# Kernel tuning notes

Measured on AMD Instinct MI355X. Metric: run time of the kernel, lower is better.

## Reference

```python
import jax, jax.numpy as jnp
import numpy as np

ATTN_DIM = 64

def setup_inputs() -> dict:
    key = jax.random.key(0)
    k1, k2, k3, k4, k5 = jax.random.split(key, 5)
    B, S, E, D = 4, 2048, 16, 256
    return {
        "input_gate": jax.random.uniform(k1, (B, S, E, 1), dtype=jnp.float32),
        "q_expert_vector": jax.random.normal(k2, (B, S, E, D), dtype=jnp.float32),
        "k_expert_vector": jax.random.normal(k3, (B, S, E, D), dtype=jnp.float32),
        "Wq": jax.random.normal(k4, (D, ATTN_DIM), dtype=jnp.float32) * 0.02,
        "Wk": jax.random.normal(k5, (D, ATTN_DIM), dtype=jnp.float32) * 0.02,
    }

def reference(input_gate, q_expert_vector, k_expert_vector, Wq, Wk):
    # project: (B,S,E,D) @ (D,A) -> (B,S,E,A)
    query = jnp.einsum("bsed,da->bsea", q_expert_vector, Wq)
    key = jnp.einsum("bsed,da->bsea", k_expert_vector, Wk)
    # attention over experts: (B,S,E,E)
    sim = jnp.einsum("bsqa,bska->bsqk", query, key) / jnp.sqrt(
        jnp.asarray(ATTN_DIM, dtype=query.dtype))
    sim = jax.nn.softmax(sim, axis=-1)
    # gate: (B,S,E,E) @ (B,S,E,1) -> (B,S,E,1)
    gate = jnp.matmul(sim, input_gate)
    routing_weight = jax.nn.softmax(gate.squeeze(-1), axis=-1)  # (B,S,E)
    return routing_weight
```

## Files before the change

kernel.cpp:

```cpp
#include <hip/hip_runtime.h>
#include <hip/hip_bf16.h>

typedef __attribute__((ext_vector_type(8))) short short8;
typedef __attribute__((ext_vector_type(4))) float f32x4;

#define WPB 8
#define BLOCK 512
#define W_PITCH 528
#define W_MAT (64 * W_PITCH)
#define QK_PITCH 144
#define QK_TILE (16 * QK_PITCH)
#define LDS_W (2 * W_MAT)
#define SCR_PW (4 * QK_TILE)
#define LDS_TOTAL (LDS_W + WPB * SCR_PW)

union S8U { short8 s; unsigned u[4]; };

__device__ __forceinline__ unsigned pk2(float a, float b) {
  __hip_bfloat162 h = __float22bfloat162_rn(make_float2(a, b));
  return *reinterpret_cast<unsigned*>(&h);
}
__device__ __forceinline__ unsigned short bf1(float a) {
  __hip_bfloat16 h = __float2bfloat16(a);
  return *reinterpret_cast<unsigned short*>(&h);
}

#define LOADX(BUF, KS) {                                                      \
  _Pragma("unroll") for (int t = 0; t < 4; ++t) {                             \
    BUF[t][0] = *(const float4*)(xr[t] + (KS) * 32);                          \
    BUF[t][1] = *(const float4*)(xr[t] + (KS) * 32 + 4);                      \
  } }

#define STEP(BUF, KS, WLDS, ACC) {                                            \
  short8 af[4];                                                               \
  _Pragma("unroll") for (int t = 0; t < 4; ++t) {                             \
    S8U u_;                                                                   \
    u_.u[0] = pk2(BUF[t][0].x, BUF[t][0].y);                                  \
    u_.u[1] = pk2(BUF[t][0].z, BUF[t][0].w);                                  \
    u_.u[2] = pk2(BUF[t][1].x, BUF[t][1].y);                                  \
    u_.u[3] = pk2(BUF[t][1].z, BUF[t][1].w);                                  \
    af[t] = u_.s;                                                             \
  }                                                                           \
  _Pragma("unroll") for (int n = 0; n < 4; ++n) {                             \
    short8 bfr = *(const short8*)((WLDS) + (n * 16 + e) * W_PITCH + (KS) * 64 + g * 16); \
    _Pragma("unroll") for (int t = 0; t < 4; ++t)                             \
      ACC[t][n] = __builtin_amdgcn_mfma_f32_16x16x32_bf16(af[t], bfr, ACC[t][n], 0, 0, 0); \
  } }

#define PROJ_PASS(XBASE, WLDS, ACC) {                                         \
  const float* xr[4];                                                         \
  _Pragma("unroll") for (int t = 0; t < 4; ++t)                               \
    xr[t] = (XBASE) + (size_t)tk[t] * 4096 + e * 256 + g * 8;                 \
  float4 b0[4][2], b1[4][2];                                                  \
  LOADX(b0, 0); LOADX(b1, 1);                                                 \
  _Pragma("unroll") for (int kp = 0; kp < 4; ++kp) {                          \
    STEP(b0, 2 * kp, WLDS, ACC);                                              \
    if (kp < 3) LOADX(b0, 2 * kp + 2);                                        \
    STEP(b1, 2 * kp + 1, WLDS, ACC);                                          \
    if (kp < 3) LOADX(b1, 2 * kp + 3);                                        \
  } }

#define WRITEQK(T, QB, KB) {                                                  \
  unsigned short* qw_ = (unsigned short*)(QB);                                \
  unsigned short* kw_ = (unsigned short*)(KB);                                \
  _Pragma("unroll") for (int n = 0; n < 4; ++n)                               \
    _Pragma("unroll") for (int r = 0; r < 4; ++r) {                           \
      int idx_ = (g * 4 + r) * 72 + n * 16 + e;                               \
      qw_[idx_] = bf1(aq[T][n][r]);                                           \
      kw_[idx_] = bf1(ak[T][n][r]);                                           \
    } }

#define ATT(T, QB, KB) {                                                      \
  f32x4 s_ = {0, 0, 0, 0};                                                    \
  _Pragma("unroll") for (int ks2 = 0; ks2 < 2; ++ks2) {                       \
    short8 fk_ = *(const short8*)((KB) + e * QK_PITCH + ks2 * 64 + g * 16);   \
    short8 fq_ = *(const short8*)((QB) + e * QK_PITCH + ks2 * 64 + g * 16);   \
    s_ = __builtin_amdgcn_mfma_f32_16x16x32_bf16(fk_, fq_, s_, 0, 0, 0);      \
  }                                                                           \
  float4 igv_ = *(const float4*)(ig + (size_t)tk[T] * 16 + g * 4);            \
  float p0_ = __expf(s_[0]), p1_ = __expf(s_[1]);                             \
  float p2_ = __expf(s_[2]), p3_ = __expf(s_[3]);                             \
  float sg_ = p0_ * igv_.x + p1_ * igv_.y + p2_ * igv_.z + p3_ * igv_.w;      \
  float se_ = (p0_ + p1_) + (p2_ + p3_);                                      \
  sg_ += __shfl_xor(sg_, 16); se_ += __shfl_xor(se_, 16);                     \
  sg_ += __shfl_xor(sg_, 32); se_ += __shfl_xor(se_, 32);                     \
  float ev_ = __expf(sg_ / se_);                                              \
  float ss_ = ev_;                                                            \
  ss_ += __shfl_xor(ss_, 1); ss_ += __shfl_xor(ss_, 2);                       \
  ss_ += __shfl_xor(ss_, 4); ss_ += __shfl_xor(ss_, 8);                       \
  if (g == 0 && wbase + (T) < ntok) out[(size_t)tk[T] * 16 + e] = ev_ / ss_;  \
}

__global__ __launch_bounds__(BLOCK, 2) void attrouter_kernel(
    const float* __restrict__ ig, const float* __restrict__ qev,
    const float* __restrict__ kev, const float* __restrict__ Wq,
    const float* __restrict__ Wk, float* __restrict__ out, int ntok)
{
  extern __shared__ char smem[];
  const int tid  = threadIdx.x;
  const int lane = tid & 63;
  const int wv   = tid >> 6;
  const int e    = lane & 15;
  const int g    = lane >> 4;

  {
    #pragma unroll
    for (int i = 0; i < 4; ++i) {
      int tile = tid + i * BLOCK;
      int m  = tile >> 10;
      int r  = tile & 1023;
      int d0 = (r >> 4) * 4;
      int a0 = (r & 15) * 4;
      const float* wsrc = m ? Wk : Wq;
      const float scl = m ? 1.0f : 0.125f;
      const float* src = wsrc + d0 * 64 + a0;
      float4 r0 = *(const float4*)(src);
      float4 r1 = *(const float4*)(src + 64);
      float4 r2 = *(const float4*)(src + 128);
      float4 r3 = *(const float4*)(src + 192);
      float c0[4] = {r0.x, r0.y, r0.z, r0.w};
      float c1[4] = {r1.x, r1.y, r1.z, r1.w};
      float c2[4] = {r2.x, r2.y, r2.z, r2.w};
      float c3[4] = {r3.x, r3.y, r3.z, r3.w};
      #pragma unroll
      for (int j = 0; j < 4; ++j) {
        uint2 v;
        v.x = pk2(scl * c0[j], scl * c1[j]);
        v.y = pk2(scl * c2[j], scl * c3[j]);
        *(uint2*)(smem + m * W_MAT + (a0 + j) * W_PITCH + d0 * 2) = v;
      }
    }
  }
  __syncthreads();

  const int wbase = (blockIdx.x * WPB + wv) * 4;
  if (wbase >= ntok) return;

  char* scr = smem + LDS_W + wv * SCR_PW;
  char* qb0 = scr;
  char* kb0 = scr + QK_TILE;
  char* qb1 = scr + 2 * QK_TILE;
  char* kb1 = scr + 3 * QK_TILE;

  int tk[4];
  #pragma unroll
  for (int t = 0; t < 4; ++t)
    tk[t] = (wbase + t < ntok) ? (wbase + t) : (ntok - 1);

  f32x4 aq[4][4] = {}; f32x4 ak[4][4] = {};

  PROJ_PASS(qev, smem, aq);
  PROJ_PASS(kev, smem + W_MAT, ak);

  WRITEQK(0, qb0, kb0);
  WRITEQK(1, qb1, kb1);
  ATT(0, qb0, kb0);
  ATT(1, qb1, kb1);
  WRITEQK(2, qb0, kb0);
  WRITEQK(3, qb1, kb1);
  ATT(2, qb0, kb0);
  ATT(3, qb1, kb1);
}

extern "C" void kernel_launch(void* const* d_in, const int* in_sizes, int n_in,
                              void* d_out, int out_size, void* d_ws, size_t ws_size,
                              hipStream_t stream) {
  const float* ig  = (const float*)d_in[0];
  const float* qev = (const float*)d_in[1];
  const float* kev = (const float*)d_in[2];
  const float* Wq  = (const float*)d_in[3];
  const float* Wk  = (const float*)d_in[4];
  float* out = (float*)d_out;
  int ntok = in_sizes[1] >> 12;

  hipFuncSetAttribute((const void*)attrouter_kernel,
                      hipFuncAttributeMaxDynamicSharedMemorySize, LDS_TOTAL);

  int grid = (ntok + WPB * 4 - 1) / (WPB * 4);
  attrouter_kernel<<<grid, BLOCK, LDS_TOTAL, stream>>>(ig, qev, kev, Wq, Wk, out, ntok);
}
```

Baseline: 52.83 us.

## Process tokens sequentially per wave with 1024-thread blocks to cut registers

```diff
diff --git a/kernel.cpp b/kernel.cpp
--- a/kernel.cpp
+++ b/kernel.cpp
@@ -4,14 +4,15 @@
 typedef __attribute__((ext_vector_type(8))) short short8;
 typedef __attribute__((ext_vector_type(4))) float f32x4;
 
-#define WPB 8
-#define BLOCK 512
+#define WPB 16
+#define BLOCK 1024
+#define TPW 2
 #define W_PITCH 528
 #define W_MAT (64 * W_PITCH)
 #define QK_PITCH 144
 #define QK_TILE (16 * QK_PITCH)
 #define LDS_W (2 * W_MAT)
-#define SCR_PW (4 * QK_TILE)
+#define SCR_PW (2 * QK_TILE)
 #define LDS_TOTAL (LDS_W + WPB * SCR_PW)
 
 union S8U { short8 s; unsigned u[4]; };
@@ -25,73 +26,37 @@
   return *reinterpret_cast<unsigned short*>(&h);
 }
 
-#define LOADX(BUF, KS) {                                                      \
-  _Pragma("unroll") for (int t = 0; t < 4; ++t) {                             \
-    BUF[t][0] = *(const float4*)(xr[t] + (KS) * 32);                          \
-    BUF[t][1] = *(const float4*)(xr[t] + (KS) * 32 + 4);                      \
+#define LOAD2(B, XROW, KS) {                                                  \
+  B[0] = *(const float4*)((XROW) + (KS) * 32);                                \
+  B[1] = *(const float4*)((XROW) + (KS) * 32 + 4); }
+
+#define STEP1(B, KS, WLDS, ACC) {                                             \
+  S8U u_;                                                                     \
+  u_.u[0] = pk2(B[0].x, B[0].y);  u_.u[1] = pk2(B[0].z, B[0].w);              \
+  u_.u[2] = pk2(B[1].x, B[1].y);  u_.u[3] = pk2(B[1].z, B[1].w);              \
+  short8 af_ = u_.s;                                                          \
+  _Pragma("unroll") for (int n = 0; n < 4; ++n) {                             \
+    short8 bf_ = *(const short8*)((WLDS) + (n * 16 + e) * W_PITCH + (KS) * 64 + g * 16); \
+    ACC[n] = __builtin_amdgcn_mfma_f32_16x16x32_bf16(af_, bf_, ACC[n], 0, 0, 0); \
   } }
 
-#define STEP(BUF, KS, WLDS, ACC) {                                            \
-  short8 af[4];                                                               \
-  _Pragma("unroll") for (int t = 0; t < 4; ++t) {                             \
-    S8U u_;                                                                   \
-    u_.u[0] = pk2(BUF[t][0].x, BUF[t][0].y);                                  \
-    u_.u[1] = pk2(BUF[t][0].z, BUF[t][0].w);                                  \
-    u_.u[2] = pk2(BUF[t][1].x, BUF[t][1].y);                                  \
-    u_.u[3] = pk2(BUF[t][1].z, BUF[t][1].w);                                  \
-    af[t] = u_.s;                                                             \
-  }                                                                           \
-  _Pragma("unroll") for (int n = 0; n < 4; ++n) {                             \
-    short8 bfr = *(const short8*)((WLDS) + (n * 16 + e) * W_PITCH + (KS) * 64 + g * 16); \
-    _Pragma("unroll") for (int t = 0; t < 4; ++t)                             \
-      ACC[t][n] = __builtin_amdgcn_mfma_f32_16x16x32_bf16(af[t], bfr, ACC[t][n], 0, 0, 0); \
+#define PROJ1(XROW, WLDS, ACC) {                                              \
+  float4 b0_[2], b1_[2];                                                      \
+  LOAD2(b0_, XROW, 0); LOAD2(b1_, XROW, 1);                                   \
+  _Pragma("unroll") for (int kp = 0; kp < 4; ++kp) {                          \
+    STEP1(b0_, 2 * kp, WLDS, ACC);                                            \
+    if (kp < 3) LOAD2(b0_, XROW, 2 * kp + 2);                                 \
+    STEP1(b1_, 2 * kp + 1, WLDS, ACC);                                        \
+    if (kp < 3) LOAD2(b1_, XROW, 2 * kp + 3);                                 \
   } }
 
-#define PROJ_PASS(XBASE, WLDS, ACC) {                                         \
-  const float* xr[4];                                                         \
-  _Pragma("unroll") for (int t = 0; t < 4; ++t)                               \
-    xr[t] = (XBASE) + (size_t)tk[t] * 4096 + e * 256 + g * 8;                 \
-  float4 b0[4][2], b1[4][2];                                                  \
-  LOADX(b0, 0); LOADX(b1, 1);                                                 \
-  _Pragma("unroll") for (int kp = 0; kp < 4; ++kp) {                          \
-    STEP(b0, 2 * kp, WLDS, ACC);                                              \
-    if (kp < 3) LOADX(b0, 2 * kp + 2);                                        \
-    STEP(b1, 2 * kp + 1, WLDS, ACC);                                          \
-    if (kp < 3) LOADX(b1, 2 * kp + 3);                                        \
-  } }
+#define WRITET(ACC, TB) {                                                     \
+  unsigned short* tw_ = (unsigned short*)(TB);                                \
+  _Pragma("unroll") for (int n = 0; n < 4; ++n)                               \
+    _Pragma("unroll") for (int r = 0; r < 4; ++r)                             \
+      tw_[(g * 4 + r) * 72 + n * 16 + e] = bf1(ACC[n][r]); }
 
-#define WRITEQK(T, QB, KB) {                                                  \
-  unsigned short* qw_ = (unsigned short*)(QB);                                \
-  unsigned short* kw_ = (unsigned short*)(KB);                                \
-  _Pragma("unroll") for (int n = 0; n < 4; ++n)                               \
-    _Pragma("unroll") for (int r = 0; r < 4; ++r) {                           \
-      int idx_ = (g * 4 + r) * 72 + n * 16 + e;                               \
-      qw_[idx_] = bf1(aq[T][n][r]);                                           \
-      kw_[idx_] = bf1(ak[T][n][r]);                                           \
-    } }
-
-#define ATT(T, QB, KB) {                                                      \
-  f32x4 s_ = {0, 0, 0, 0};                                                    \
-  _Pragma("unroll") for (int ks2 = 0; ks2 < 2; ++ks2) {                       \
-    short8 fk_ = *(const short8*)((KB) + e * QK_PITCH + ks2 * 64 + g * 16);   \
-    short8 fq_ = *(const short8*)((QB) + e * QK_PITCH + ks2 * 64 + g * 16);   \
-    s_ = __builtin_amdgcn_mfma_f32_16x16x32_bf16(fk_, fq_, s_, 0, 0, 0);      \
-  }                                                                           \
-  float4 igv_ = *(const float4*)(ig + (size_t)tk[T] * 16 + g * 4);            \
-  float p0_ = __expf(s_[0]), p1_ = __expf(s_[1]);                             \
-  float p2_ = __expf(s_[2]), p3_ = __expf(s_[3]);                             \
-  float sg_ = p0_ * igv_.x + p1_ * igv_.y + p2_ * igv_.z + p3_ * igv_.w;      \
-  float se_ = (p0_ + p1_) + (p2_ + p3_);                                      \
-  sg_ += __shfl_xor(sg_, 16); se_ += __shfl_xor(se_, 16);                     \
-  sg_ += __shfl_xor(sg_, 32); se_ += __shfl_xor(se_, 32);                     \
-  float ev_ = __expf(sg_ / se_);                                              \
-  float ss_ = ev_;                                                            \
-  ss_ += __shfl_xor(ss_, 1); ss_ += __shfl_xor(ss_, 2);                       \
-  ss_ += __shfl_xor(ss_, 4); ss_ += __shfl_xor(ss_, 8);                       \
-  if (g == 0 && wbase + (T) < ntok) out[(size_t)tk[T] * 16 + e] = ev_ / ss_;  \
-}
-
-__global__ __launch_bounds__(BLOCK, 2) void attrouter_kernel(
+__global__ __launch_bounds__(BLOCK) void attrouter_kernel(
     const float* __restrict__ ig, const float* __restrict__ qev,
     const float* __restrict__ kev, const float* __restrict__ Wq,
     const float* __restrict__ Wk, float* __restrict__ out, int ntok)
@@ -105,7 +70,7 @@
 
   {
     #pragma unroll
-    for (int i = 0; i < 4; ++i) {
+    for (int i = 0; i < 2; ++i) {
       int tile = tid + i * BLOCK;
       int m  = tile >> 10;
       int r  = tile & 1023;
@@ -133,33 +98,47 @@
   }
   __syncthreads();
 
-  const int wbase = (blockIdx.x * WPB + wv) * 4;
-  if (wbase >= ntok) return;
+  char* qt = smem + LDS_W + wv * SCR_PW;
+  char* kt = qt + QK_TILE;
 
-  char* scr = smem + LDS_W + wv * SCR_PW;
-  char* qb0 = scr;
-  char* kb0 = scr + QK_TILE;
-  char* qb1 = scr + 2 * QK_TILE;
-  char* kb1 = scr + 3 * QK_TILE;
+  const int wbase = (blockIdx.x * WPB + wv) * TPW;
 
-  int tk[4];
   #pragma unroll
-  for (int t = 0; t < 4; ++t)
-    tk[t] = (wbase + t < ntok) ? (wbase + t) : (ntok - 1);
+  for (int t = 0; t < TPW; ++t) {
+    const int tok = wbase + t;
+    if (tok >= ntok) break;
+    const float* qrow = qev + (size_t)tok * 4096 + e * 256 + g * 8;
+    const float* krow = kev + (size_t)tok * 4096 + e * 256 + g * 8;
 
-  f32x4 aq[4][4] = {}; f32x4 ak[4][4] = {};
+    f32x4 aq[4] = {{0,0,0,0},{0,0,0,0},{0,0,0,0},{0,0,0,0}};
+    PROJ1(qrow, smem, aq);
+    WRITET(aq, qt);
 
-  PROJ_PASS(qev, smem, aq);
-  PROJ_PASS(kev, smem + W_MAT, ak);
+    f32x4 ak[4] = {{0,0,0,0},{0,0,0,0},{0,0,0,0},{0,0,0,0}};
+    PROJ1(krow, smem + W_MAT, ak);
+    WRITET(ak, kt);
 
-  WRITEQK(0, qb0, kb0);
-  WRITEQK(1, qb1, kb1);
-  ATT(0, qb0, kb0);
-  ATT(1, qb1, kb1);
-  WRITEQK(2, qb0, kb0);
-  WRITEQK(3, qb1, kb1);
-  ATT(2, qb0, kb0);
-  ATT(3, qb1, kb1);
+    short8 fq0 = *(const short8*)(qt + e * QK_PITCH + g * 16);
+    short8 fq1 = *(const short8*)(qt + e * QK_PITCH + 64 + g * 16);
+    short8 fk0 = *(const short8*)(kt + e * QK_PITCH + g * 16);
+    short8 fk1 = *(const short8*)(kt + e * QK_PITCH + 64 + g * 16);
+    f32x4 s = {0, 0, 0, 0};
+    s = __builtin_amdgcn_mfma_f32_16x16x32_bf16(fk0, fq0, s, 0, 0, 0);
+    s = __builtin_amdgcn_mfma_f32_16x16x32_bf16(fk1, fq1, s, 0, 0, 0);
+
+    float4 igv = *(const float4*)(ig + (size_t)tok * 16 + g * 4);
+    float p0 = __expf(s[0]), p1 = __expf(s[1]);
+    float p2 = __expf(s[2]), p3 = __expf(s[3]);
+    float sg = p0 * igv.x + p1 * igv.y + p2 * igv.z + p3 * igv.w;
+    float se = (p0 + p1) + (p2 + p3);
+    sg += __shfl_xor(sg, 16); se += __shfl_xor(se, 16);
+    sg += __shfl_xor(sg, 32); se += __shfl_xor(se, 32);
+    float ev = __expf(sg / se);
+    float ss = ev;
+    ss += __shfl_xor(ss, 1); ss += __shfl_xor(ss, 2);
+    ss += __shfl_xor(ss, 4); ss += __shfl_xor(ss, 8);
+    if (g == 0) out[(size_t)tok * 16 + e] = ev / ss;
+  }
 }
 
 extern "C" void kernel_launch(void* const* d_in, const int* in_sizes, int n_in,
@@ -176,6 +155,6 @@
   hipFuncSetAttribute((const void*)attrouter_kernel,
                       hipFuncAttributeMaxDynamicSharedMemorySize, LDS_TOTAL);
 
-  int grid = (ntok + WPB * 4 - 1) / (WPB * 4);
+  int grid = (ntok + WPB * TPW - 1) / (WPB * TPW);
   attrouter_kernel<<<grid, BLOCK, LDS_TOTAL, stream>>>(ig, qev, kev, Wq, Wk, out, ntok);
 }
```

Measured after the change: 49.58 us. 6.1% less time.
